# Optimization experiments

Hardware: AMD Instinct MI355X
Metric: run time of the kernel (lower is better)

Reference implementation:

```python
import jax, jax.numpy as jnp
import numpy as np

C = 256          # channels
K = 7            # involution kernel size
GC = 16          # group_channels (fixed in source)
G = C // GC      # groups = 16
RED = C // 4     # reduction channels = 64
B, H, W = 4, 56, 56


def setup_inputs() -> dict:
    key = jax.random.key(0)
    k0, k1, k2 = jax.random.split(key, 3)
    x = jax.random.normal(k0, (B, C, H, W), jnp.float32)
    w1 = jax.random.normal(k1, (RED, C), jnp.float32) * (1.0 / np.sqrt(C))
    b1 = jnp.zeros((RED,), jnp.float32)
    w2 = jax.random.normal(k2, (K * K * G, RED), jnp.float32) * (1.0 / np.sqrt(RED))
    b2 = jnp.zeros((K * K * G,), jnp.float32)
    return {"x": x, "w1": w1, "b1": b1, "w2": w2, "b2": b2}


def reference(x, w1, b1, w2, b2):
    b, c, h, w = x.shape
    # 1x1 conv generator: conv1 (C -> C/4) + ReLU, conv2 (C/4 -> K^2*G)
    t = jax.nn.relu(jnp.einsum('bchw,oc->bohw', x, w1) + b1[None, :, None, None])
    weight = jnp.einsum('bohw,ko->bkhw', t, w2) + b2[None, :, None, None]
    weight = weight.reshape(b, G, K * K, h, w)             # (b, G, K^2, h, w)
    # unfold: patches ordered (C, kh, kw) channel-slowest, matching torch.nn.Unfold
    pad = (K - 1) // 2
    patches = jax.lax.conv_general_dilated_patches(
        x, (K, K), (1, 1), [(pad, pad), (pad, pad)],
        dimension_numbers=('NCHW', 'OIHW', 'NCHW'))        # (b, C*K*K, h, w)
    patches = patches.reshape(b, G, GC, K * K, h, w)
    # per-pixel, per-group weighted sum over the K^2 window positions
    out = jnp.einsum('bgkhw,bgckhw->bgchw', weight, patches)
    return out.reshape(b, c, h, w)
```

## Files before the change

### kernel.cpp

```cpp
#include <hip/hip_runtime.h>

#define B_    4
#define C_    256
#define Kk    7
#define GC_   16
#define G_    16
#define RED_  64
#define H_    56
#define W_    56
#define HW_   3136
#define KK_   49
#define KG_   784
#define NP_   12544

typedef float  f4    __attribute__((ext_vector_type(4)));
typedef float  f32x4 __attribute__((ext_vector_type(4)));
typedef __bf16 bf16x8 __attribute__((ext_vector_type(8)));
typedef __bf16 bf16x4 __attribute__((ext_vector_type(4)));
typedef unsigned short u16;
typedef u16    u16x4 __attribute__((ext_vector_type(4)));

__device__ __forceinline__ f4 ld4(const float* p) { return *(const f4*)p; }
__device__ __forceinline__ void st4(float* p, f4 v) { *(f4*)p = v; }
__device__ __forceinline__ float bf2f(u16 u) {
    return __uint_as_float(((unsigned)u) << 16);
}

__global__ __launch_bounds__(256) void xt_kernel(const float* __restrict__ x,
                                                 __bf16* __restrict__ xt) {
    __shared__ __bf16 lt[64][68];
    const int tid = threadIdx.x;
    const int P0  = blockIdx.x * 64;
    const int c0  = blockIdx.y * 64;
    const int b   = P0 / HW_;
    const int p0  = P0 - b * HW_;

    const int pq  = tid & 15;
    const int crb = tid >> 4;
#pragma unroll
    for (int i = 0; i < 4; ++i) {
        const int cr = crb + i * 16;
        const f4 v = ld4(x + (size_t)(b * C_ + c0 + cr) * HW_ + p0 + pq * 4);
#pragma unroll
        for (int j = 0; j < 4; ++j) lt[pq * 4 + j][cr] = (__bf16)v[j];
    }
    __syncthreads();
    const int cq  = tid & 15;
    const int plb = tid >> 4;
#pragma unroll
    for (int i = 0; i < 4; ++i) {
        const int pl = plb + i * 16;
        const bf16x4 rv = *(const bf16x4*)&lt[pl][cq * 4];
        *(bf16x4*)(xt + (size_t)(P0 + pl) * C_ + c0 + cq * 4) = rv;
    }
}

__global__ __launch_bounds__(256) void gen1m2(const __bf16* __restrict__ xt,
                                              const float* __restrict__ w1,
                                              const float* __restrict__ b1,
                                              __bf16* __restrict__ t) {
    __shared__ __bf16 w1s[64][260];
    const int tid  = threadIdx.x;
    const int lane = tid & 63;
    const int wave = tid >> 6;
    const int row  = lane & 15;
    const int kg   = lane >> 4;
    const int P0w  = blockIdx.x * 64 + wave * 16;

    const __bf16* bp = xt + (size_t)(P0w + row) * C_ + kg * 8;
    bf16x8 bv[8];
#pragma unroll
    for (int ks = 0; ks < 8; ++ks) bv[ks] = *(const bf16x8*)(bp + ks * 32);

#pragma unroll
    for (int i = 0; i < 16; ++i) {
        const int q  = tid + i * 256;
        const int r  = q >> 6;
        const int c0 = (q & 63) * 4;
        const f4 v = ld4(w1 + (size_t)r * C_ + c0);
        bf16x4 pk;
#pragma unroll
        for (int j = 0; j < 4; ++j) pk[j] = (__bf16)v[j];
        *(bf16x4*)&w1s[r][c0] = pk;
    }
    __syncthreads();

    f32x4 acc[4] = {f32x4(0.f), f32x4(0.f), f32x4(0.f), f32x4(0.f)};
#pragma unroll
    for (int ks = 0; ks < 8; ++ks)
#pragma unroll
        for (int mt = 0; mt < 4; ++mt) {
            const bf16x8 af = *(const bf16x8*)&w1s[mt * 16 + row][ks * 32 + kg * 8];
            acc[mt] = __builtin_amdgcn_mfma_f32_16x16x32_bf16(af, bv[ks], acc[mt], 0, 0, 0);
        }

#pragma unroll
    for (int mt = 0; mt < 4; ++mt) {
        const f4 bias = ld4(b1 + mt * 16 + kg * 4);
        bf16x4 pk;
#pragma unroll
        for (int j = 0; j < 4; ++j)
            pk[j] = (__bf16)fmaxf(acc[mt][j] + bias[j], 0.f);
        *(bf16x4*)(t + (size_t)(P0w + row) * RED_ + mt * 16 + kg * 4) = pk;
    }
}

__global__ __launch_bounds__(256) void gen2_mfma2(const __bf16* __restrict__ t,
                                                  const float* __restrict__ w2,
                                                  const float* __restrict__ b2,
                                                  __bf16* __restrict__ wgt) {
    __shared__ __bf16 w2s[64][68];
    const int tid  = threadIdx.x;
    const int lane = tid & 63;
    const int wave = tid >> 6;
    const int row  = lane & 15;
    const int kg   = lane >> 4;
    const int P0   = blockIdx.x * 256 + wave * 64;
    const int k0   = blockIdx.y * 64;
    const int nMt  = (blockIdx.y == 12) ? 1 : 4;

    bf16x8 bfrag[4][2];
#pragma unroll
    for (int cg = 0; cg < 4; ++cg)
#pragma unroll
        for (int ks = 0; ks < 2; ++ks)
            bfrag[cg][ks] = *(const bf16x8*)(t + (size_t)(P0 + cg * 16 + row) * RED_
                                               + ks * 32 + kg * 8);

#pragma unroll
    for (int i = 0; i < 4; ++i) {
        const int q  = tid + i * 256;
        const int r  = q >> 4;
        const int c0 = (q & 15) * 4;
        f4 v = {0.f, 0.f, 0.f, 0.f};
        if (k0 + r < KG_) v = ld4(w2 + (size_t)(k0 + r) * RED_ + c0);
        bf16x4 pk;
#pragma unroll
        for (int j = 0; j < 4; ++j) pk[j] = (__bf16)v[j];
        *(bf16x4*)&w2s[r][c0] = pk;
    }
    __syncthreads();

    for (int mt = 0; mt < nMt; ++mt) {
        const bf16x8 afr0 = *(const bf16x8*)&w2s[mt * 16 + row][kg * 8];
        const bf16x8 afr1 = *(const bf16x8*)&w2s[mt * 16 + row][32 + kg * 8];
        f32x4 acc[4] = {f32x4(0.f), f32x4(0.f), f32x4(0.f), f32x4(0.f)};
#pragma unroll
        for (int cg = 0; cg < 4; ++cg) {
            acc[cg] = __builtin_amdgcn_mfma_f32_16x16x32_bf16(afr0, bfrag[cg][0], acc[cg], 0, 0, 0);
            acc[cg] = __builtin_amdgcn_mfma_f32_16x16x32_bf16(afr1, bfrag[cg][1], acc[cg], 0, 0, 0);
        }
        const f4 bias = ld4(b2 + k0 + mt * 16 + kg * 4);
#pragma unroll
        for (int cg = 0; cg < 4; ++cg) {
            const int Pcg = P0 + cg * 16;
            const int b   = Pcg / HW_;
            const int p   = Pcg - b * HW_ + row;
            const size_t base = ((size_t)b * KG_ + (size_t)(k0 + mt * 16 + kg * 4)) * HW_ + p;
#pragma unroll
            for (int j = 0; j < 4; ++j)
                wgt[base + (size_t)j * HW_] = (__bf16)(acc[cg][j] + bias[j]);
        }
    }
}

#define BR_  4
#define XR_  10
#define XST_ 68
__global__ __launch_bounds__(256) void inv_kernel(const float* __restrict__ x,
                                                  const u16* __restrict__ wgt,
                                                  float* __restrict__ out) {
    __shared__ float xs[GC_][XR_][XST_];
    __shared__ u16   wsm[KK_][BR_][W_];
    const int tid = threadIdx.x;
    const int r0  = blockIdx.x * BR_;
    const int g   = blockIdx.y;
    const int b   = blockIdx.z;

    for (int idx = tid; idx < GC_ * XR_ * 16; idx += 256) {
        const int c   = idx / (XR_ * 16);
        const int rem = idx - c * (XR_ * 16);
        const int hr  = rem >> 4;
        const int wq  = rem & 15;
        const int h   = r0 - 3 + hr;
        f4 v = {0.f, 0.f, 0.f, 0.f};
        if (h >= 0 && h < H_) {
            const float* xr_ = x + (size_t)(b * C_ + g * GC_ + c) * HW_ + h * W_;
            const int w0 = wq * 4 - 3;
            if (wq >= 1 && wq <= 13) {
                v = ld4(xr_ + w0);
            } else {
#pragma unroll
                for (int j = 0; j < 4; ++j) {
                    const int w = w0 + j;
                    if (w >= 0 && w < W_) v[j] = xr_[w];
                }
            }
        }
        *(f4*)&xs[c][hr][wq * 4] = v;
    }
    for (int idx = tid; idx < KK_ * BR_ * 14; idx += 256) {
        const int k   = idx / (BR_ * 14);
        const int rem = idx - k * (BR_ * 14);
        const int r   = rem / 14;
        const int cq  = rem - r * 14;
        const u16x4 v = *(const u16x4*)(wgt + ((size_t)b * KG_ + (size_t)g * KK_ + k) * HW_
                                            + (r0 + r) * W_ + cq * 4);
        *(u16x4*)&wsm[k][r][cq * 4] = v;
    }
    __syncthreads();

    if (tid >= 224) return;
    const int cq  = tid % 14;
    const int r   = (tid / 14) & 3;
    const int cg4 = tid / 56;

    f4 acc[4] = {f4(0.f), f4(0.f), f4(0.f), f4(0.f)};
#pragma unroll
    for (int kh = 0; kh < Kk; ++kh) {
        float tf[7][4];
#pragma unroll
        for (int kw = 0; kw < 7; ++kw) {
            const u16x4 tv = *(const u16x4*)&wsm[kh * 7 + kw][r][cq * 4];
#pragma unroll
            for (int j = 0; j < 4; ++j) tf[kw][j] = bf2f(tv[j]);
        }
        const int hr = r + kh;
#pragma unroll
        for (int ci = 0; ci < 4; ++ci) {
            const float* xrow = &xs[cg4 * 4 + ci][hr][cq * 4];
            const f4 x0 = ld4(xrow), x1 = ld4(xrow + 4), x2 = ld4(xrow + 8);
            float xw[12];
#pragma unroll
            for (int j = 0; j < 4; ++j) { xw[j] = x0[j]; xw[4 + j] = x1[j]; xw[8 + j] = x2[j]; }
#pragma unroll
            for (int kw = 0; kw < 7; ++kw)
#pragma unroll
                for (int j = 0; j < 4; ++j)
                    acc[ci][j] = fmaf(tf[kw][j], xw[j + kw], acc[ci][j]);
        }
    }

#pragma unroll
    for (int ci = 0; ci < 4; ++ci)
        st4(out + (size_t)(b * C_ + g * GC_ + cg4 * 4 + ci) * HW_ + (r0 + r) * W_ + cq * 4,
            acc[ci]);
}

extern "C" void kernel_launch(void* const* d_in, const int* in_sizes, int n_in,
                              void* d_out, int out_size, void* d_ws, size_t ws_size,
                              hipStream_t stream) {
    const float* x  = (const float*)d_in[0];
    const float* w1 = (const float*)d_in[1];
    const float* b1 = (const float*)d_in[2];
    const float* w2 = (const float*)d_in[3];
    const float* b2 = (const float*)d_in[4];
    float* out = (float*)d_out;

    char* ws = (char*)d_ws;
    __bf16* xt  = (__bf16*)ws;
    __bf16* t   = (__bf16*)(ws + (size_t)NP_ * C_ * 2);
    __bf16* wgt = (__bf16*)(ws + (size_t)NP_ * C_ * 2 + (size_t)NP_ * RED_ * 2);

    xt_kernel  <<<dim3(NP_ / 64, C_ / 64), 256, 0, stream>>>(x, xt);
    gen1m2     <<<dim3(NP_ / 64),          256, 0, stream>>>(xt, w1, b1, t);
    gen2_mfma2 <<<dim3(NP_ / 256, 13),     256, 0, stream>>>(t, w2, b2, wgt);
    inv_kernel <<<dim3(14, G_, B_),        256, 0, stream>>>(x, (const u16*)wgt, out);
}
```

Measured before the change: 121.5 us.

## Stage gen2 output through LDS for vector stores; store x tile as bf16

The weight-generation kernel now writes its MFMA results into a per-wave LDS tile and then emits 16-byte row stores to the weight tensor, replacing scattered 2-byte stores. The involution kernel stores its x halo tile in LDS as bf16 instead of fp32, halving LDS footprint and read traffic, and loads the weights with 8-wide vectors. The bf16 x tile adds rounding error to the input activations, and the per-wave 64-pixel tile assumes no batch boundary falls inside a wave's pixel range.

```diff
diff --git a/kernel.cpp b/kernel.cpp
--- a/kernel.cpp
+++ b/kernel.cpp
@@ -19,6 +19,7 @@
 typedef __bf16 bf16x4 __attribute__((ext_vector_type(4)));
 typedef unsigned short u16;
 typedef u16    u16x4 __attribute__((ext_vector_type(4)));
+typedef u16    u16x8 __attribute__((ext_vector_type(8)));
 
 __device__ __forceinline__ f4 ld4(const float* p) { return *(const f4*)p; }
 __device__ __forceinline__ void st4(float* p, f4 v) { *(f4*)p = v; }
@@ -105,17 +106,20 @@
     }
 }
 
-__global__ __launch_bounds__(256) void gen2_mfma2(const __bf16* __restrict__ t,
+__global__ __launch_bounds__(256) void gen2_mfma3(const __bf16* __restrict__ t,
                                                   const float* __restrict__ w2,
                                                   const float* __restrict__ b2,
                                                   __bf16* __restrict__ wgt) {
     __shared__ __bf16 w2s[64][68];
+    __shared__ u16    sw[4][16][72];
     const int tid  = threadIdx.x;
     const int lane = tid & 63;
     const int wave = tid >> 6;
     const int row  = lane & 15;
     const int kg   = lane >> 4;
-    const int P0   = blockIdx.x * 256 + wave * 64;
+    const int Pw   = blockIdx.x * 256 + wave * 64;
+    const int b    = Pw / HW_;
+    const int pw   = Pw - b * HW_;
     const int k0   = blockIdx.y * 64;
     const int nMt  = (blockIdx.y == 12) ? 1 : 4;
 
@@ -124,7 +128,7 @@
     for (int cg = 0; cg < 4; ++cg)
 #pragma unroll
         for (int ks = 0; ks < 2; ++ks)
-            bfrag[cg][ks] = *(const bf16x8*)(t + (size_t)(P0 + cg * 16 + row) * RED_
+            bfrag[cg][ks] = *(const bf16x8*)(t + (size_t)(Pw + cg * 16 + row) * RED_
                                                + ks * 32 + kg * 8);
 
 #pragma unroll
@@ -152,61 +156,72 @@
         }
         const f4 bias = ld4(b2 + k0 + mt * 16 + kg * 4);
 #pragma unroll
-        for (int cg = 0; cg < 4; ++cg) {
-            const int Pcg = P0 + cg * 16;
-            const int b   = Pcg / HW_;
-            const int p   = Pcg - b * HW_ + row;
-            const size_t base = ((size_t)b * KG_ + (size_t)(k0 + mt * 16 + kg * 4)) * HW_ + p;
-#pragma unroll
-            for (int j = 0; j < 4; ++j)
-                wgt[base + (size_t)j * HW_] = (__bf16)(acc[cg][j] + bias[j]);
-        }
-    }
-}
-
-#define BR_  4
-#define XR_  10
-#define XST_ 68
+        for (int cg = 0; cg < 4; ++cg)
+#pragma unroll
+            for (int j = 0; j < 4; ++j) {
+                const __bf16 v = (__bf16)(acc[cg][j] + bias[j]);
+                sw[wave][kg * 4 + j][cg * 16 + row] = *(const u16*)&v;
+            }
+#pragma unroll
+        for (int u = 0; u < 2; ++u) {
+            const int r16 = (lane >> 3) + u * 8;
+            const int ch  = lane & 7;
+            const u16x8 v = *(const u16x8*)&sw[wave][r16][ch * 8];
+            *(u16x8*)((u16*)wgt + ((size_t)b * KG_ + k0 + mt * 16 + r16) * HW_
+                                + pw + ch * 8) = v;
+        }
+    }
+}
+
+#define BR_   4
+#define XR_   10
+#define XPW_  72
 __global__ __launch_bounds__(256) void inv_kernel(const float* __restrict__ x,
                                                   const u16* __restrict__ wgt,
                                                   float* __restrict__ out) {
-    __shared__ float xs[GC_][XR_][XST_];
-    __shared__ u16   wsm[KK_][BR_][W_];
+    __shared__ u16 xs[GC_][XR_][XPW_];
+    __shared__ u16 wsm[KK_][BR_][W_];
     const int tid = threadIdx.x;
     const int r0  = blockIdx.x * BR_;
     const int g   = blockIdx.y;
     const int b   = blockIdx.z;
 
-    for (int idx = tid; idx < GC_ * XR_ * 16; idx += 256) {
-        const int c   = idx / (XR_ * 16);
-        const int rem = idx - c * (XR_ * 16);
-        const int hr  = rem >> 4;
-        const int wq  = rem & 15;
+    for (int idx = tid; idx < GC_ * XR_ * 18; idx += 256) {
+        const int c   = idx / (XR_ * 18);
+        const int rem = idx - c * (XR_ * 18);
+        const int hr  = rem / 18;
+        const int qd  = rem - hr * 18;
         const int h   = r0 - 3 + hr;
+        const int px0 = qd * 4 - 3;
         f4 v = {0.f, 0.f, 0.f, 0.f};
         if (h >= 0 && h < H_) {
             const float* xr_ = x + (size_t)(b * C_ + g * GC_ + c) * HW_ + h * W_;
-            const int w0 = wq * 4 - 3;
-            if (wq >= 1 && wq <= 13) {
-                v = ld4(xr_ + w0);
+            if (qd >= 1 && qd <= 13) {
+                v = ld4(xr_ + px0);
             } else {
 #pragma unroll
                 for (int j = 0; j < 4; ++j) {
-                    const int w = w0 + j;
-                    if (w >= 0 && w < W_) v[j] = xr_[w];
+                    const int px = px0 + j;
+                    if (px >= 0 && px < W_) v[j] = xr_[px];
                 }
             }
         }
-        *(f4*)&xs[c][hr][wq * 4] = v;
-    }
-    for (int idx = tid; idx < KK_ * BR_ * 14; idx += 256) {
-        const int k   = idx / (BR_ * 14);
-        const int rem = idx - k * (BR_ * 14);
-        const int r   = rem / 14;
-        const int cq  = rem - r * 14;
-        const u16x4 v = *(const u16x4*)(wgt + ((size_t)b * KG_ + (size_t)g * KK_ + k) * HW_
-                                            + (r0 + r) * W_ + cq * 4);
-        *(u16x4*)&wsm[k][r][cq * 4] = v;
+        u16x4 pk;
+#pragma unroll
+        for (int j = 0; j < 4; ++j) {
+            const __bf16 bv = (__bf16)v[j];
+            pk[j] = *(const u16*)&bv;
+        }
+        *(u16x4*)&xs[c][hr][qd * 4] = pk;
+    }
+    for (int idx = tid; idx < KK_ * BR_ * 7; idx += 256) {
+        const int k   = idx / (BR_ * 7);
+        const int rem = idx - k * (BR_ * 7);
+        const int r   = rem / 7;
+        const int ch  = rem - r * 7;
+        const u16x8 v = *(const u16x8*)(wgt + ((size_t)b * KG_ + (size_t)g * KK_ + k) * HW_
+                                            + (r0 + r) * W_ + ch * 8);
+        *(u16x8*)&wsm[k][r][ch * 8] = v;
     }
     __syncthreads();
 
@@ -228,11 +243,14 @@
         const int hr = r + kh;
 #pragma unroll
         for (int ci = 0; ci < 4; ++ci) {
-            const float* xrow = &xs[cg4 * 4 + ci][hr][cq * 4];
-            const f4 x0 = ld4(xrow), x1 = ld4(xrow + 4), x2 = ld4(xrow + 8);
+            const u16* xrow = &xs[cg4 * 4 + ci][hr][cq * 4];
             float xw[12];
 #pragma unroll
-            for (int j = 0; j < 4; ++j) { xw[j] = x0[j]; xw[4 + j] = x1[j]; xw[8 + j] = x2[j]; }
+            for (int q = 0; q < 3; ++q) {
+                const u16x4 xv = *(const u16x4*)(xrow + q * 4);
+#pragma unroll
+                for (int j = 0; j < 4; ++j) xw[q * 4 + j] = bf2f(xv[j]);
+            }
 #pragma unroll
             for (int kw = 0; kw < 7; ++kw)
 #pragma unroll
@@ -264,6 +282,6 @@
 
     xt_kernel  <<<dim3(NP_ / 64, C_ / 64), 256, 0, stream>>>(x, xt);
     gen1m2     <<<dim3(NP_ / 64),          256, 0, stream>>>(xt, w1, b1, t);
-    gen2_mfma2 <<<dim3(NP_ / 256, 13),     256, 0, stream>>>(t, w2, b2, wgt);
+    gen2_mfma3 <<<dim3(NP_ / 256, 13),     256, 0, stream>>>(t, w2, b2, wgt);
     inv_kernel <<<dim3(14, G_, B_),        256, 0, stream>>>(x, (const u16*)wgt, out);
 }
```

After: 153.6 us. 26.4% more time.
